# Optimization experiments

Measured on AMD Instinct MI355X. Metric: run time of the kernel, lower is better.

The kernel has to match this reference:

```python
import jax, jax.numpy as jnp
import numpy as np

D_IN = 1024
D_OUT = 1024

def setup_inputs() -> dict:
    key = jax.random.key(0)
    ks = jax.random.split(key, 7)
    s = 1.0 / np.sqrt(D_IN)
    x = jax.random.normal(ks[0], (4, 2048, D_IN), dtype=jnp.float32)
    Wq = jax.random.uniform(ks[1], (D_IN, D_OUT), jnp.float32, -s, s)
    bq = jax.random.uniform(ks[2], (D_OUT,), jnp.float32, -s, s)
    Wk = jax.random.uniform(ks[3], (D_IN, D_OUT), jnp.float32, -s, s)
    bk = jax.random.uniform(ks[4], (D_OUT,), jnp.float32, -s, s)
    Wv = jax.random.uniform(ks[5], (D_IN, D_OUT), jnp.float32, -s, s)
    bv = jax.random.uniform(ks[6], (D_OUT,), jnp.float32, -s, s)
    return {"x": x, "Wq": Wq, "bq": bq, "Wk": Wk, "bk": bk, "Wv": Wv, "bv": bv}

def reference(x, Wq, bq, Wk, bk, Wv, bv):
    # q,k,v: [B, T, d_out]
    q = x @ Wq + bq
    k = x @ Wk + bk
    v = x @ Wv + bv
    T = x.shape[1]
    scale = 1.0 / jnp.sqrt(jnp.asarray(D_OUT, x.dtype))
    qk = jnp.einsum('btd,bsd->bts', q, k) * scale  # [B, T, T]
    causal = jnp.tril(jnp.ones((T, T), dtype=bool))
    qk = jnp.where(causal, qk, -jnp.inf)
    probs = jax.nn.softmax(qk, axis=-1)
    return jnp.einsum('bts,bsd->btd', probs, v)
```

## Files before the change

kernel.cpp:

```cpp
#include <hip/hip_runtime.h>
#include <cstdint>
#include <cmath>

#define D_MODEL 1024
#define SEQ 2048
#define BATCH 4

typedef short bf16x8 __attribute__((ext_vector_type(8)));
typedef float f32x4 __attribute__((ext_vector_type(4)));

__device__ __forceinline__ short f2bf(float f) {
  union { float f; unsigned int u; } v; v.f = f;
  unsigned int r = (v.u + 0x7FFFu + ((v.u >> 16) & 1u)) >> 16;
  return (short)r;
}

__device__ __forceinline__ float bf2f(short h) {
  union { unsigned int u; float f; } v;
  v.u = ((unsigned int)(unsigned short)h) << 16;
  return v.f;
}

__device__ __forceinline__ f32x4 mfma16(bf16x8 a, bf16x8 b, f32x4 c) {
  return __builtin_amdgcn_mfma_f32_16x16x32_bf16(a, b, c, 0, 0, 0);
}

__device__ __forceinline__ void load_lds16(const void* g, void* l) {
  __builtin_amdgcn_global_load_lds(
      (const __attribute__((address_space(1))) unsigned int*)g,
      (__attribute__((address_space(3))) unsigned int*)l, 16, 0, 0);
}

__global__ __launch_bounds__(256) void convert_x(const float* __restrict__ x,
                                                 short* __restrict__ xb) {
  int i = blockIdx.x * 256 + threadIdx.x;
  float4 f = ((const float4*)x)[i];
  short4 h;
  h.x = f2bf(f.x); h.y = f2bf(f.y); h.z = f2bf(f.z); h.w = f2bf(f.w);
  ((short4*)xb)[i] = h;
}

__global__ __launch_bounds__(256) void transpose_w(const float* __restrict__ Wq,
                                                   const float* __restrict__ Wk,
                                                   const float* __restrict__ Wv,
                                                   short* __restrict__ wt) {
  const int mat = blockIdx.z;
  const float* __restrict__ W = (mat == 0) ? Wq : (mat == 1) ? Wk : Wv;
  short* __restrict__ o = wt + (size_t)mat * (D_MODEL * D_MODEL);
  __shared__ float tile[32][33];
  const int k0 = blockIdx.x * 32, n0 = blockIdx.y * 32;
  const int lx = threadIdx.x & 31, ly = threadIdx.x >> 5;
#pragma unroll
  for (int i = 0; i < 4; ++i) {
    int r = ly + i * 8;
    tile[r][lx] = W[(size_t)(k0 + r) * D_MODEL + n0 + lx];
  }
  __syncthreads();
#pragma unroll
  for (int i = 0; i < 4; ++i) {
    int r = ly + i * 8;
    o[(size_t)(n0 + r) * D_MODEL + k0 + lx] = f2bf(tile[lx][r]);
  }
}

__global__ __launch_bounds__(512, 4) void qkv_gemm(
    const short* __restrict__ xb, const short* __restrict__ wt,
    const float* __restrict__ bq, const float* __restrict__ bk,
    const float* __restrict__ bv, short* __restrict__ qo,
    short* __restrict__ ko, short* __restrict__ vo) {
  const int m0 = blockIdx.x * 256;
  const int n0 = blockIdx.y * 128;
  const int mat = blockIdx.z;
  const short* __restrict__ w = wt + (size_t)mat * (D_MODEL * D_MODEL);
  const float* __restrict__ bias = (mat == 0) ? bq : (mat == 1) ? bk : bv;

  __shared__ short a_lds[2][256 * 32];
  __shared__ short b_lds[2][128 * 32];

  const int tid = threadIdx.x;
  const int wid = tid >> 6;
  const int lane = tid & 63;
  const int quad = lane >> 4;
  const int l16 = lane & 15;
  const int wm = (wid >> 1) * 64;
  const int wn = (wid & 1) * 64;
  const int key = (l16 >> 1) & 3;

  f32x4 acc[4][4] = {};

  auto stage = [&](int k0, int buf) {
#pragma unroll
    for (int h = 0; h < 2; ++h) {
      const int c = tid + h * 512;
      load_lds16(xb + (size_t)(m0 + (c >> 2)) * D_MODEL + k0 +
                     (((c & 3) ^ ((c >> 3) & 3)) << 3),
                 (char*)&a_lds[buf][c * 8]);
    }
    load_lds16(w + (size_t)(n0 + (tid >> 2)) * D_MODEL + k0 +
                   (((tid & 3) ^ ((tid >> 3) & 3)) << 3),
               (char*)&b_lds[buf][tid * 8]);
  };

  stage(0, 0);
  for (int k0 = 0; k0 < D_MODEL; k0 += 32) {
    const int buf = (k0 >> 5) & 1;
    __syncthreads();
    if (k0 + 32 < D_MODEL) stage(k0 + 32, buf ^ 1);
    const short* al = a_lds[buf];
    const short* bl = b_lds[buf];
    bf16x8 af[4], bfr[4];
#pragma unroll
    for (int i = 0; i < 4; ++i)
      af[i] = *(const bf16x8*)(al + (wm + i * 16 + l16) * 32 +
                               ((quad ^ key) << 3));
#pragma unroll
    for (int j = 0; j < 4; ++j)
      bfr[j] = *(const bf16x8*)(bl + (wn + j * 16 + l16) * 32 +
                                ((quad ^ key) << 3));
#pragma unroll
    for (int i = 0; i < 4; ++i)
#pragma unroll
      for (int j = 0; j < 4; ++j)
        acc[i][j] = mfma16(af[i], bfr[j], acc[i][j]);
  }
#pragma unroll
  for (int i = 0; i < 4; ++i) {
#pragma unroll
    for (int j = 0; j < 4; ++j) {
#pragma unroll
      for (int r = 0; r < 4; ++r) {
        const int mrow = m0 + wm + i * 16 + quad * 4 + r;
        const int ncol = n0 + wn + j * 16 + l16;
        const float val = acc[i][j][r] + bias[ncol];
        const short h = f2bf(val);
        if (mat == 2) {
          const int bb = mrow >> 11;
          const int t = mrow & 2047;
          vo[((size_t)bb * D_MODEL + ncol) * SEQ + t] = h;
        } else if (mat == 0) {
          qo[(size_t)mrow * D_MODEL + ncol] = h;
        } else {
          ko[(size_t)mrow * D_MODEL + ncol] = h;
        }
      }
    }
  }
}

__global__ __launch_bounds__(256) void sgemm(const short* __restrict__ qb,
                                             const short* __restrict__ kb,
                                             short* __restrict__ S) {
  if (blockIdx.y > blockIdx.x) return;
  const int m0 = blockIdx.x * 128;
  const int n0 = blockIdx.y * 128;
  const int b = blockIdx.z;
  const short* __restrict__ qp = qb + (size_t)b * SEQ * D_MODEL;
  const short* __restrict__ kp = kb + (size_t)b * SEQ * D_MODEL;

  __shared__ short a_lds[2][128 * 64];
  __shared__ short b_lds[2][128 * 64];

  const int tid = threadIdx.x;
  const int wid = tid >> 6;
  const int lane = tid & 63;
  const int quad = lane >> 4;
  const int l16 = lane & 15;
  const int mw = (wid >> 1) * 64;
  const int nw = (wid & 1) * 64;
  const int sw = l16 & 7;
  const int r_local = wid * 8 + (lane >> 3);
  const int c_sw = ((lane & 7) ^ (lane >> 3)) * 8;

  f32x4 acc[4][4] = {};

  auto stage = [&](int k0, int buf) {
#pragma unroll
    for (int it = 0; it < 4; ++it) {
      load_lds16(qp + (size_t)(m0 + it * 32 + r_local) * D_MODEL + k0 + c_sw,
                 (char*)a_lds[buf] + it * 4096 + wid * 1024);
      load_lds16(kp + (size_t)(n0 + it * 32 + r_local) * D_MODEL + k0 + c_sw,
                 (char*)b_lds[buf] + it * 4096 + wid * 1024);
    }
  };

  stage(0, 0);
  for (int k0 = 0; k0 < D_MODEL; k0 += 64) {
    const int buf = (k0 >> 6) & 1;
    __syncthreads();
    if (k0 + 64 < D_MODEL) stage(k0 + 64, buf ^ 1);
    const short* al = a_lds[buf];
    const short* bl = b_lds[buf];
#pragma unroll
    for (int kt = 0; kt < 2; ++kt) {
      bf16x8 af[4], bfr[4];
#pragma unroll
      for (int i = 0; i < 4; ++i)
        af[i] = *(const bf16x8*)(al + (mw + i * 16 + l16) * 64 +
                                 ((kt * 4 + quad) ^ sw) * 8);
#pragma unroll
      for (int i = 0; i < 4; ++i)
        bfr[i] = *(const bf16x8*)(bl + (nw + i * 16 + l16) * 64 +
                                  ((kt * 4 + quad) ^ sw) * 8);
#pragma unroll
      for (int i = 0; i < 4; ++i)
#pragma unroll
        for (int j = 0; j < 4; ++j)
          acc[i][j] = mfma16(af[i], bfr[j], acc[i][j]);
    }
  }
#pragma unroll
  for (int i = 0; i < 4; ++i) {
#pragma unroll
    for (int j = 0; j < 4; ++j) {
#pragma unroll
      for (int r = 0; r < 4; ++r) {
        const int mrow = m0 + mw + i * 16 + quad * 4 + r;
        const int ncol = n0 + nw + j * 16 + l16;
        S[((size_t)b * SEQ + mrow) * SEQ + ncol] = f2bf(acc[i][j][r] * 0.03125f);
      }
    }
  }
}

__global__ __launch_bounds__(256) void softmax_rows(const short* __restrict__ S,
                                                    short* __restrict__ P) {
  const int row = blockIdx.x;
  const int t = row & (SEQ - 1);
  const int tid = threadIdx.x;
  const short* __restrict__ srow = S + (size_t)row * SEQ;
  short* __restrict__ prow = P + (size_t)row * SEQ;

  __shared__ float red[4];

  float v[8];
#pragma unroll
  for (int i = 0; i < 8; ++i) {
    const int c = tid + i * 256;
    v[i] = (c <= t) ? bf2f(srow[c]) : -1e30f;
  }
  float m = v[0];
#pragma unroll
  for (int i = 1; i < 8; ++i) m = fmaxf(m, v[i]);
#pragma unroll
  for (int o = 32; o; o >>= 1) m = fmaxf(m, __shfl_xor(m, o));
  if ((tid & 63) == 0) red[tid >> 6] = m;
  __syncthreads();
  m = fmaxf(fmaxf(red[0], red[1]), fmaxf(red[2], red[3]));

  float e[8];
  float s = 0.f;
#pragma unroll
  for (int i = 0; i < 8; ++i) {
    e[i] = __expf(v[i] - m);
    s += e[i];
  }
#pragma unroll
  for (int o = 32; o; o >>= 1) s += __shfl_xor(s, o);
  __syncthreads();
  if ((tid & 63) == 0) red[tid >> 6] = s;
  __syncthreads();
  s = red[0] + red[1] + red[2] + red[3];
  const float rinv = 1.0f / s;
  const int nwr = (t >> 8) + 1;
#pragma unroll
  for (int i = 0; i < 8; ++i)
    if (i < nwr) prow[tid + i * 256] = f2bf(e[i] * rinv);
}

__global__ __launch_bounds__(256) void pvgemm(const short* __restrict__ P,
                                              const short* __restrict__ vtb,
                                              float* __restrict__ out) {
  const int n0 = blockIdx.x * 128;
  const int b = blockIdx.y;
  const int m0 = (15 - blockIdx.z) * 128;
  const short* __restrict__ pp = P + (size_t)b * SEQ * SEQ;
  const short* __restrict__ vp = vtb + (size_t)b * D_MODEL * SEQ;
  const int kmax = m0 + 128;

  __shared__ short a_lds[2][128 * 64];
  __shared__ short b_lds[2][128 * 64];

  const int tid = threadIdx.x;
  const int wid = tid >> 6;
  const int lane = tid & 63;
  const int quad = lane >> 4;
  const int l16 = lane & 15;
  const int mw = (wid >> 1) * 64;
  const int nw = (wid & 1) * 64;
  const int sw = l16 & 7;
  const int r_local = wid * 8 + (lane >> 3);
  const int c_sw = ((lane & 7) ^ (lane >> 3)) * 8;

  f32x4 acc[4][4] = {};

  auto stage = [&](int k0, int buf) {
#pragma unroll
    for (int it = 0; it < 4; ++it) {
      load_lds16(pp + (size_t)(m0 + it * 32 + r_local) * SEQ + k0 + c_sw,
                 (char*)a_lds[buf] + it * 4096 + wid * 1024);
      load_lds16(vp + (size_t)(n0 + it * 32 + r_local) * SEQ + k0 + c_sw,
                 (char*)b_lds[buf] + it * 4096 + wid * 1024);
    }
  };

  stage(0, 0);
  for (int k0 = 0; k0 < kmax; k0 += 64) {
    const int buf = (k0 >> 6) & 1;
    __syncthreads();
    if (k0 + 64 < kmax) stage(k0 + 64, buf ^ 1);
    const short* al = a_lds[buf];
    const short* bl = b_lds[buf];
#pragma unroll
    for (int kt = 0; kt < 2; ++kt) {
      bf16x8 af[4], bfr[4];
#pragma unroll
      for (int i = 0; i < 4; ++i)
        af[i] = *(const bf16x8*)(al + (mw + i * 16 + l16) * 64 +
                                 ((kt * 4 + quad) ^ sw) * 8);
#pragma unroll
      for (int i = 0; i < 4; ++i)
        bfr[i] = *(const bf16x8*)(bl + (nw + i * 16 + l16) * 64 +
                                  ((kt * 4 + quad) ^ sw) * 8);
#pragma unroll
      for (int i = 0; i < 4; ++i)
#pragma unroll
        for (int j = 0; j < 4; ++j)
          acc[i][j] = mfma16(af[i], bfr[j], acc[i][j]);
    }
  }
#pragma unroll
  for (int i = 0; i < 4; ++i) {
#pragma unroll
    for (int j = 0; j < 4; ++j) {
#pragma unroll
      for (int r = 0; r < 4; ++r) {
        const int mrow = m0 + mw + i * 16 + quad * 4 + r;
        const int ncol = n0 + nw + j * 16 + l16;
        out[((size_t)b * SEQ + mrow) * D_MODEL + ncol] = acc[i][j][r];
      }
    }
  }
}

extern "C" void kernel_launch(void* const* d_in, const int* in_sizes, int n_in,
                              void* d_out, int out_size, void* d_ws, size_t ws_size,
                              hipStream_t stream) {
  (void)in_sizes; (void)n_in; (void)out_size; (void)ws_size;
  const float* x  = (const float*)d_in[0];
  const float* Wq = (const float*)d_in[1];
  const float* bq = (const float*)d_in[2];
  const float* Wk = (const float*)d_in[3];
  const float* bk = (const float*)d_in[4];
  const float* Wv = (const float*)d_in[5];
  const float* bv = (const float*)d_in[6];
  float* out = (float*)d_out;

  char* ws = (char*)d_ws;
  short* xb = (short*)(ws);
  short* wt = (short*)(ws + 16777216);
  short* qo = (short*)(ws + 23068672);
  short* ko = (short*)(ws + 39845888);
  short* vo = (short*)(ws + 56623104);
  short* S  = (short*)(ws + 73400320);
  short* P  = (short*)(ws);

  convert_x<<<dim3(8192), dim3(256), 0, stream>>>(x, xb);
  transpose_w<<<dim3(32, 32, 3), dim3(256), 0, stream>>>(Wq, Wk, Wv, wt);
  qkv_gemm<<<dim3(32, 8, 3), dim3(512), 0, stream>>>(xb, wt, bq, bk, bv, qo, ko, vo);
  sgemm<<<dim3(16, 16, BATCH), dim3(256), 0, stream>>>(qo, ko, S);
  softmax_rows<<<dim3(BATCH * SEQ), dim3(256), 0, stream>>>(S, P);
  pvgemm<<<dim3(8, BATCH, 16), dim3(256), 0, stream>>>(P, vo, out);
}
```

Measured before the change: 263.3 us.

## Merge prep kernels, triangular sgemm grid, and halve GEMM K-tile to 32

```diff
diff --git a/kernel.cpp b/kernel.cpp
--- a/kernel.cpp
+++ b/kernel.cpp
@@ -31,24 +31,29 @@
       (__attribute__((address_space(3))) unsigned int*)l, 16, 0, 0);
 }
 
-__global__ __launch_bounds__(256) void convert_x(const float* __restrict__ x,
-                                                 short* __restrict__ xb) {
-  int i = blockIdx.x * 256 + threadIdx.x;
-  float4 f = ((const float4*)x)[i];
-  short4 h;
-  h.x = f2bf(f.x); h.y = f2bf(f.y); h.z = f2bf(f.z); h.w = f2bf(f.w);
-  ((short4*)xb)[i] = h;
-}
-
-__global__ __launch_bounds__(256) void transpose_w(const float* __restrict__ Wq,
-                                                   const float* __restrict__ Wk,
-                                                   const float* __restrict__ Wv,
-                                                   short* __restrict__ wt) {
-  const int mat = blockIdx.z;
+__global__ __launch_bounds__(256) void prep(const float* __restrict__ x,
+                                            const float* __restrict__ Wq,
+                                            const float* __restrict__ Wk,
+                                            const float* __restrict__ Wv,
+                                            short* __restrict__ xb,
+                                            short* __restrict__ wt) {
+  const int bx = blockIdx.x;
+  if (bx < 8192) {
+    const int i = bx * 256 + threadIdx.x;
+    float4 f = ((const float4*)x)[i];
+    short4 h;
+    h.x = f2bf(f.x); h.y = f2bf(f.y); h.z = f2bf(f.z); h.w = f2bf(f.w);
+    ((short4*)xb)[i] = h;
+    return;
+  }
+  const int b2 = bx - 8192;
+  const int mat = b2 >> 10;
+  const int rem = b2 & 1023;
+  const int k0 = (rem & 31) * 32;
+  const int n0 = (rem >> 5) * 32;
   const float* __restrict__ W = (mat == 0) ? Wq : (mat == 1) ? Wk : Wv;
   short* __restrict__ o = wt + (size_t)mat * (D_MODEL * D_MODEL);
   __shared__ float tile[32][33];
-  const int k0 = blockIdx.x * 32, n0 = blockIdx.y * 32;
   const int lx = threadIdx.x & 31, ly = threadIdx.x >> 5;
 #pragma unroll
   for (int i = 0; i < 4; ++i) {
@@ -150,15 +155,18 @@
 __global__ __launch_bounds__(256) void sgemm(const short* __restrict__ qb,
                                              const short* __restrict__ kb,
                                              short* __restrict__ S) {
-  if (blockIdx.y > blockIdx.x) return;
-  const int m0 = blockIdx.x * 128;
-  const int n0 = blockIdx.y * 128;
-  const int b = blockIdx.z;
+  const int t = blockIdx.x;
+  int r = (int)((sqrtf(8.0f * t + 1.0f) - 1.0f) * 0.5f);
+  while ((r + 1) * (r + 2) / 2 <= t) ++r;
+  while (r * (r + 1) / 2 > t) --r;
+  const int m0 = r * 128;
+  const int n0 = (t - r * (r + 1) / 2) * 128;
+  const int b = blockIdx.y;
   const short* __restrict__ qp = qb + (size_t)b * SEQ * D_MODEL;
   const short* __restrict__ kp = kb + (size_t)b * SEQ * D_MODEL;
 
-  __shared__ short a_lds[2][128 * 64];
-  __shared__ short b_lds[2][128 * 64];
+  __shared__ short a_lds[2][128 * 32];
+  __shared__ short b_lds[2][128 * 32];
 
   const int tid = threadIdx.x;
   const int wid = tid >> 6;
@@ -167,56 +175,53 @@
   const int l16 = lane & 15;
   const int mw = (wid >> 1) * 64;
   const int nw = (wid & 1) * 64;
-  const int sw = l16 & 7;
-  const int r_local = wid * 8 + (lane >> 3);
-  const int c_sw = ((lane & 7) ^ (lane >> 3)) * 8;
+  const int key = (l16 >> 1) & 3;
 
   f32x4 acc[4][4] = {};
 
   auto stage = [&](int k0, int buf) {
 #pragma unroll
-    for (int it = 0; it < 4; ++it) {
-      load_lds16(qp + (size_t)(m0 + it * 32 + r_local) * D_MODEL + k0 + c_sw,
-                 (char*)a_lds[buf] + it * 4096 + wid * 1024);
-      load_lds16(kp + (size_t)(n0 + it * 32 + r_local) * D_MODEL + k0 + c_sw,
-                 (char*)b_lds[buf] + it * 4096 + wid * 1024);
+    for (int h = 0; h < 2; ++h) {
+      const int c = tid + h * 256;
+      const int gc = ((c & 3) ^ ((c >> 3) & 3)) << 3;
+      load_lds16(qp + (size_t)(m0 + (c >> 2)) * D_MODEL + k0 + gc,
+                 (char*)&a_lds[buf][c * 8]);
+      load_lds16(kp + (size_t)(n0 + (c >> 2)) * D_MODEL + k0 + gc,
+                 (char*)&b_lds[buf][c * 8]);
     }
   };
 
   stage(0, 0);
-  for (int k0 = 0; k0 < D_MODEL; k0 += 64) {
-    const int buf = (k0 >> 6) & 1;
+  for (int k0 = 0; k0 < D_MODEL; k0 += 32) {
+    const int buf = (k0 >> 5) & 1;
     __syncthreads();
-    if (k0 + 64 < D_MODEL) stage(k0 + 64, buf ^ 1);
+    if (k0 + 32 < D_MODEL) stage(k0 + 32, buf ^ 1);
     const short* al = a_lds[buf];
     const short* bl = b_lds[buf];
-#pragma unroll
-    for (int kt = 0; kt < 2; ++kt) {
-      bf16x8 af[4], bfr[4];
-#pragma unroll
-      for (int i = 0; i < 4; ++i)
-        af[i] = *(const bf16x8*)(al + (mw + i * 16 + l16) * 64 +
-                                 ((kt * 4 + quad) ^ sw) * 8);
-#pragma unroll
-      for (int i = 0; i < 4; ++i)
-        bfr[i] = *(const bf16x8*)(bl + (nw + i * 16 + l16) * 64 +
-                                  ((kt * 4 + quad) ^ sw) * 8);
-#pragma unroll
-      for (int i = 0; i < 4; ++i)
-#pragma unroll
-        for (int j = 0; j < 4; ++j)
-          acc[i][j] = mfma16(af[i], bfr[j], acc[i][j]);
-    }
+    bf16x8 af[4], bfr[4];
+#pragma unroll
+    for (int i = 0; i < 4; ++i)
+      af[i] = *(const bf16x8*)(al + (mw + i * 16 + l16) * 32 +
+                               ((quad ^ key) << 3));
+#pragma unroll
+    for (int j = 0; j < 4; ++j)
+      bfr[j] = *(const bf16x8*)(bl + (nw + j * 16 + l16) * 32 +
+                                ((quad ^ key) << 3));
+#pragma unroll
+    for (int i = 0; i < 4; ++i)
+#pragma unroll
+      for (int j = 0; j < 4; ++j)
+        acc[i][j] = mfma16(af[i], bfr[j], acc[i][j]);
   }
 #pragma unroll
   for (int i = 0; i < 4; ++i) {
 #pragma unroll
     for (int j = 0; j < 4; ++j) {
 #pragma unroll
-      for (int r = 0; r < 4; ++r) {
-        const int mrow = m0 + mw + i * 16 + quad * 4 + r;
+      for (int rr = 0; rr < 4; ++rr) {
+        const int mrow = m0 + mw + i * 16 + quad * 4 + rr;
         const int ncol = n0 + nw + j * 16 + l16;
-        S[((size_t)b * SEQ + mrow) * SEQ + ncol] = f2bf(acc[i][j][r] * 0.03125f);
+        S[((size_t)b * SEQ + mrow) * SEQ + ncol] = f2bf(acc[i][j][rr] * 0.03125f);
       }
     }
   }
@@ -236,7 +241,8 @@
 #pragma unroll
   for (int i = 0; i < 8; ++i) {
     const int c = tid + i * 256;
-    v[i] = (c <= t) ? bf2f(srow[c]) : -1e30f;
+    v[i] = -1e30f;
+    if (c <= t) v[i] = bf2f(srow[c]);
   }
   float m = v[0];
 #pragma unroll
@@ -277,8 +283,8 @@
   const short* __restrict__ vp = vtb + (size_t)b * D_MODEL * SEQ;
   const int kmax = m0 + 128;
 
-  __shared__ short a_lds[2][128 * 64];
-  __shared__ short b_lds[2][128 * 64];
+  __shared__ short a_lds[2][128 * 32];
+  __shared__ short b_lds[2][128 * 32];
 
   const int tid = threadIdx.x;
   const int wid = tid >> 6;
@@ -287,46 +293,43 @@
   const int l16 = lane & 15;
   const int mw = (wid >> 1) * 64;
   const int nw = (wid & 1) * 64;
-  const int sw = l16 & 7;
-  const int r_local = wid * 8 + (lane >> 3);
-  const int c_sw = ((lane & 7) ^ (lane >> 3)) * 8;
+  const int key = (l16 >> 1) & 3;
 
   f32x4 acc[4][4] = {};
 
   auto stage = [&](int k0, int buf) {
 #pragma unroll
-    for (int it = 0; it < 4; ++it) {
-      load_lds16(pp + (size_t)(m0 + it * 32 + r_local) * SEQ + k0 + c_sw,
-                 (char*)a_lds[buf] + it * 4096 + wid * 1024);
-      load_lds16(vp + (size_t)(n0 + it * 32 + r_local) * SEQ + k0 + c_sw,
-                 (char*)b_lds[buf] + it * 4096 + wid * 1024);
+    for (int h = 0; h < 2; ++h) {
+      const int c = tid + h * 256;
+      const int gc = ((c & 3) ^ ((c >> 3) & 3)) << 3;
+      load_lds16(pp + (size_t)(m0 + (c >> 2)) * SEQ + k0 + gc,
+                 (char*)&a_lds[buf][c * 8]);
+      load_lds16(vp + (size_t)(n0 + (c >> 2)) * SEQ + k0 + gc,
+                 (char*)&b_lds[buf][c * 8]);
     }
   };
 
   stage(0, 0);
-  for (int k0 = 0; k0 < kmax; k0 += 64) {
-    const int buf = (k0 >> 6) & 1;
+  for (int k0 = 0; k0 < kmax; k0 += 32) {
+    const int buf = (k0 >> 5) & 1;
     __syncthreads();
-    if (k0 + 64 < kmax) stage(k0 + 64, buf ^ 1);
+    if (k0 + 32 < kmax) stage(k0 + 32, buf ^ 1);
     const short* al = a_lds[buf];
     const short* bl = b_lds[buf];
-#pragma unroll
-    for (int kt = 0; kt < 2; ++kt) {
-      bf16x8 af[4], bfr[4];
-#pragma unroll
-      for (int i = 0; i < 4; ++i)
-        af[i] = *(const bf16x8*)(al + (mw + i * 16 + l16) * 64 +
-                                 ((kt * 4 + quad) ^ sw) * 8);
-#pragma unroll
-      for (int i = 0; i < 4; ++i)
-        bfr[i] = *(const bf16x8*)(bl + (nw + i * 16 + l16) * 64 +
-                                  ((kt * 4 + quad) ^ sw) * 8);
-#pragma unroll
-      for (int i = 0; i < 4; ++i)
-#pragma unroll
-        for (int j = 0; j < 4; ++j)
-          acc[i][j] = mfma16(af[i], bfr[j], acc[i][j]);
-    }
+    bf16x8 af[4], bfr[4];
+#pragma unroll
+    for (int i = 0; i < 4; ++i)
+      af[i] = *(const bf16x8*)(al + (mw + i * 16 + l16) * 32 +
+                               ((quad ^ key) << 3));
+#pragma unroll
+    for (int j = 0; j < 4; ++j)
+      bfr[j] = *(const bf16x8*)(bl + (nw + j * 16 + l16) * 32 +
+                                ((quad ^ key) << 3));
+#pragma unroll
+    for (int i = 0; i < 4; ++i)
+#pragma unroll
+      for (int j = 0; j < 4; ++j)
+        acc[i][j] = mfma16(af[i], bfr[j], acc[i][j]);
   }
 #pragma unroll
   for (int i = 0; i < 4; ++i) {
@@ -364,10 +367,9 @@
   short* S  = (short*)(ws + 73400320);
   short* P  = (short*)(ws);
 
-  convert_x<<<dim3(8192), dim3(256), 0, stream>>>(x, xb);
-  transpose_w<<<dim3(32, 32, 3), dim3(256), 0, stream>>>(Wq, Wk, Wv, wt);
+  prep<<<dim3(8192 + 3072), dim3(256), 0, stream>>>(x, Wq, Wk, Wv, xb, wt);
   qkv_gemm<<<dim3(32, 8, 3), dim3(512), 0, stream>>>(xb, wt, bq, bk, bv, qo, ko, vo);
-  sgemm<<<dim3(16, 16, BATCH), dim3(256), 0, stream>>>(qo, ko, S);
+  sgemm<<<dim3(136, BATCH), dim3(256), 0, stream>>>(qo, ko, S);
   softmax_rows<<<dim3(BATCH * SEQ), dim3(256), 0, stream>>>(S, P);
   pvgemm<<<dim3(8, BATCH, 16), dim3(256), 0, stream>>>(P, vo, out);
 }
```

After: 268.0 us. Within noise of the previous version (+1.8%).
